# Kernel tuning notes

Measured on AMD Instinct MI355X. Metric: run time of the kernel, lower is better.

Reference implementation:

```python
import jax, jax.numpy as jnp
import numpy as np

NUM_FIELDS = 26

def setup_inputs() -> dict:
    key = jax.random.key(0)
    ks = jax.random.split(key, 8)
    B, F, D, V, d, af = 4096, NUM_FIELDS, 13, 100000, 64, 64
    return {
        "sparse_feat": jax.random.randint(ks[0], (B, F), 0, V, dtype=jnp.int32),
        "dense_feat": jax.random.uniform(ks[1], (B, D), dtype=jnp.float32),
        "embed_table": jax.random.normal(ks[2], (V, d), dtype=jnp.float32) * 0.05,
        "lin_table": jax.random.normal(ks[3], (V,), dtype=jnp.float32) * 0.05,
        "w_dense": jax.random.normal(ks[4], (D,), dtype=jnp.float32) * 0.1,
        "bias": jnp.zeros((1,), dtype=jnp.float32),
        "W1": jax.random.normal(ks[5], (d, af), dtype=jnp.float32) * (1.0 / np.sqrt(d)),
        "b1": jnp.zeros((af,), dtype=jnp.float32),
        "w2": jax.random.normal(ks[6], (af,), dtype=jnp.float32) * (1.0 / np.sqrt(af)),
        "p": jax.random.normal(ks[7], (d,), dtype=jnp.float32) * (1.0 / np.sqrt(d)),
    }

def reference(sparse_feat, dense_feat, embed_table, lin_table, w_dense, bias, W1, b1, w2, p):
    # Embedding lookup: [B, F, d]
    emb = embed_table[sparse_feat]
    # Linear part: per-field scalar weights + dense linear + bias -> [B]
    linear_out = lin_table[sparse_feat].sum(axis=1) + dense_feat @ w_dense + bias[0]
    # Pairwise interactions i<j (static indices): [B, P, d]
    i_idx, j_idx = np.triu_indices(NUM_FIELDS, k=1)
    att_x = emb[:, i_idx, :] * emb[:, j_idx, :]
    # Attention MLP: Linear(d, af) + ReLU + Linear(af, 1, no bias) -> [B, P]
    h = jax.nn.relu(jnp.einsum('bpd,da->bpa', att_x, W1) + b1)
    att_w = jnp.einsum('bpa,a->bp', h, w2)
    att_score = jax.nn.softmax(att_w, axis=1)
    # Softmax-weighted sum over pairs -> [B, d], then final projection p -> [B]
    att_out = jnp.einsum('bpd,bp->bd', att_x, att_score)
    fm_att_out = att_out @ p
    return linear_out + fm_att_out
```

## Files before the change

kernel.cpp:

```cpp
#include <hip/hip_runtime.h>
#include <math.h>


#define NF 26
#define NP 325
#define NMT 21
#define ED 64
#define AF 64
#define NDENSE 13
#define WPB 4
#define BLOCK (WPB * 64)
#define ESTRIDE 72
#define WSTRIDE 72

typedef __attribute__((ext_vector_type(8))) _Float16 half8;
typedef __attribute__((ext_vector_type(4))) float f32x4;

__device__ __forceinline__ half8 bcast8(float v) {
    _Float16 hh = (_Float16)v;
    half8 r = { hh, hh, hh, hh, hh, hh, hh, hh };
    return r;
}

__device__ __forceinline__ float qd_sum(float x) {
#if __has_builtin(__builtin_amdgcn_permlane16_swap) && __has_builtin(__builtin_amdgcn_permlane32_swap)
    {
        auto a = __builtin_amdgcn_permlane16_swap(__builtin_bit_cast(unsigned, x),
                                                  __builtin_bit_cast(unsigned, x),
                                                  false, false);
        x = __builtin_bit_cast(float, a[0]) + __builtin_bit_cast(float, a[1]);
        auto b = __builtin_amdgcn_permlane32_swap(__builtin_bit_cast(unsigned, x),
                                                  __builtin_bit_cast(unsigned, x),
                                                  false, false);
        x = __builtin_bit_cast(float, b[0]) + __builtin_bit_cast(float, b[1]);
    }
#else
    x += __shfl_xor(x, 16, 64);
    x += __shfl_xor(x, 32, 64);
#endif
    return x;
}

__global__ __launch_bounds__(BLOCK, 2)
void afm_kernel(const int*   __restrict__ sparse,
                const float* __restrict__ dense,
                const float* __restrict__ etab,
                const float* __restrict__ ltab,
                const float* __restrict__ wdense,
                const float* __restrict__ bias,
                const float* __restrict__ W1,
                const float* __restrict__ b1,
                const float* __restrict__ w2,
                const float* __restrict__ proj,
                float*       __restrict__ out,
                int B)
{
    const int t    = threadIdx.x;
    const int wave = t >> 6;
    const int lane = t & 63;
    const int qd   = lane >> 4;
    const int ln   = lane & 15;

    __shared__ alignas(16) _Float16       w1t_s[AF][WSTRIDE];
    __shared__              unsigned short tab_s[NMT * 16];
    __shared__ alignas(16) _Float16       emb_all[WPB][NF][ESTRIDE];

    for (int task = t; task < WPB * NF * 8; task += BLOCK) {
        int w   = task / (NF * 8);
        int rem = task - w * (NF * 8);
        int f = rem >> 3, c = rem & 7;
        int rw = blockIdx.x * WPB + w;
        if (rw < B) {
            const float* src = etab + (size_t)sparse[rw * NF + f] * ED + c * 8;
            float4 v0 = *(const float4*)(src);
            float4 v1 = *(const float4*)(src + 4);
            half8 hv = { (_Float16)v0.x, (_Float16)v0.y, (_Float16)v0.z, (_Float16)v0.w,
                         (_Float16)v1.x, (_Float16)v1.y, (_Float16)v1.z, (_Float16)v1.w };
            *(half8*)(&emb_all[w][f][c * 8]) = hv;
        }
    }
    for (int idx = t; idx < ED * AF; idx += BLOCK) {
        int d = idx >> 6, a = idx & 63;
        w1t_s[a][d] = (_Float16)W1[idx];
    }
    for (int p = t; p < NMT * 16; p += BLOCK) {
        unsigned short v = 0;
        if (p < NP) {
            int rem = p, i = 0;
            while (rem >= NF - 1 - i) { rem -= NF - 1 - i; ++i; }
            v = (unsigned short)(i | ((i + 1 + rem) << 8));
        }
        tab_s[p] = v;
    }

    const int r = blockIdx.x * WPB + wave;
    const bool active = (r < B);

    _Float16 (* __restrict__ emb)[ESTRIDE] = emb_all[wave];

    __syncthreads();
    if (!active) return;

    float4 b1v4[4], w2v4[4];
    #pragma unroll
    for (int nt = 0; nt < 4; ++nt) {
        b1v4[nt] = *(const float4*)(b1 + nt * 16 + qd * 4);
        w2v4[nt] = *(const float4*)(w2 + nt * 16 + qd * 4);
    }

    half8 bfr[4][2];
    #pragma unroll
    for (int nt = 0; nt < 4; ++nt)
        #pragma unroll
        for (int kh = 0; kh < 2; ++kh)
            bfr[nt][kh] = *(const half8*)(&w1t_s[nt * 16 + ln][kh * 32 + qd * 8]);

    float m = -INFINITY, l = 0.f;
    half8 acc0 = bcast8(0.f), acc1 = bcast8(0.f);

    {
        unsigned pp = tab_s[ln];
        int fi = pp & 0xff, fj = pp >> 8;
        (void)fi; (void)fj;
    }
    unsigned pp0 = tab_s[ln];
    int fi0 = pp0 & 0xff, fj0 = pp0 >> 8;
    half8 eiR0 = *(const half8*)(&emb[fi0][qd * 8]);
    half8 eiR1 = *(const half8*)(&emb[fi0][32 + qd * 8]);
    half8 ejR0 = *(const half8*)(&emb[fj0][qd * 8]);
    half8 ejR1 = *(const half8*)(&emb[fj0][32 + qd * 8]);

    float lgP = 0.f;
    half8 xP0 = bcast8(0.f), xP1 = bcast8(0.f);

    for (int k = 0; k < NMT; ++k) {
        half8 xC0 = eiR0 * ejR0;
        half8 xC1 = eiR1 * ejR1;

        if (k + 1 < NMT) {
            unsigned np = tab_s[(k + 1) * 16 + ln];
            int nfi = np & 0xff, nfj = np >> 8;
            eiR0 = *(const half8*)(&emb[nfi][qd * 8]);
            eiR1 = *(const half8*)(&emb[nfi][32 + qd * 8]);
            ejR0 = *(const half8*)(&emb[nfj][qd * 8]);
            ejR1 = *(const half8*)(&emb[nfj][32 + qd * 8]);
        }

        float lgp[4];
        #pragma unroll
        for (int nt = 0; nt < 4; ++nt) {
            f32x4 acc = { b1v4[nt].x, b1v4[nt].y, b1v4[nt].z, b1v4[nt].w };
            acc = __builtin_amdgcn_mfma_f32_16x16x32_f16(bfr[nt][0], xC0, acc, 0, 0, 0);
            acc = __builtin_amdgcn_mfma_f32_16x16x32_f16(bfr[nt][1], xC1, acc, 0, 0, 0);
            float u = fmaf(fmaxf(acc[1], 0.f), w2v4[nt].y, fmaxf(acc[0], 0.f) * w2v4[nt].x);
            float v = fmaf(fmaxf(acc[3], 0.f), w2v4[nt].w, fmaxf(acc[2], 0.f) * w2v4[nt].z);
            lgp[nt] = u + v;
        }
        float lg = (lgp[0] + lgp[1]) + (lgp[2] + lgp[3]);
        lg = qd_sum(lg);
        if (k * 16 + ln >= NP) lg = -INFINITY;

        if (k > 0) {
            float mn    = fmaxf(m, lgP);
            float alpha = __expf(m - mn);
            float e     = __expf(lgP - mn);
            l = l * alpha + e;
            m = mn;
            half8 a8 = bcast8(alpha), e8 = bcast8(e);
            acc0 = acc0 * a8 + xP0 * e8;
            acc1 = acc1 * a8 + xP1 * e8;
        }
        xP0 = xC0; xP1 = xC1; lgP = lg;
    }
    {
        float mn    = fmaxf(m, lgP);
        float alpha = __expf(m - mn);
        float e     = __expf(lgP - mn);
        l = l * alpha + e;
        m = mn;
        half8 a8 = bcast8(alpha), e8 = bcast8(e);
        acc0 = acc0 * a8 + xP0 * e8;
        acc1 = acc1 * a8 + xP1 * e8;
    }

    float lin = 0.f;
    if (lane < NF) {
        lin = ltab[sparse[r * NF + lane]];
    } else if (lane >= 32 && lane < 32 + NDENSE) {
        int k = lane - 32;
        lin = dense[r * NDENSE + k] * wdense[k];
    }
    #pragma unroll
    for (int off = 32; off >= 1; off >>= 1) lin += __shfl_xor(lin, off, 64);
    lin += bias[0];

    float mg = m;
    #pragma unroll
    for (int off = 1; off <= 8; off <<= 1) mg = fmaxf(mg, __shfl_xor(mg, off, 64));
    const float fac = __expf(m - mg);
    float lsum = l * fac;
    #pragma unroll
    for (int off = 1; off <= 8; off <<= 1) lsum += __shfl_xor(lsum, off, 64);

    float4 pa4 = *(const float4*)(proj + qd * 8);
    float4 pb4 = *(const float4*)(proj + qd * 8 + 4);
    float4 pc4 = *(const float4*)(proj + 32 + qd * 8);
    float4 pd4 = *(const float4*)(proj + 32 + qd * 8 + 4);
    float rr = (float)acc0[0] * pa4.x + (float)acc0[1] * pa4.y
             + (float)acc0[2] * pa4.z + (float)acc0[3] * pa4.w
             + (float)acc0[4] * pb4.x + (float)acc0[5] * pb4.y
             + (float)acc0[6] * pb4.z + (float)acc0[7] * pb4.w
             + (float)acc1[0] * pc4.x + (float)acc1[1] * pc4.y
             + (float)acc1[2] * pc4.z + (float)acc1[3] * pc4.w
             + (float)acc1[4] * pd4.x + (float)acc1[5] * pd4.y
             + (float)acc1[6] * pd4.z + (float)acc1[7] * pd4.w;
    rr *= fac;
    #pragma unroll
    for (int off = 1; off <= 32; off <<= 1) rr += __shfl_xor(rr, off, 64);

    if (lane == 0) out[r] = lin + rr / lsum;
}

extern "C" void kernel_launch(void* const* d_in, const int* in_sizes, int n_in,
                              void* d_out, int out_size, void* d_ws, size_t ws_size,
                              hipStream_t stream) {
    const int*   sparse = (const int*)  d_in[0];
    const float* dense  = (const float*)d_in[1];
    const float* etab   = (const float*)d_in[2];
    const float* ltab   = (const float*)d_in[3];
    const float* wdense = (const float*)d_in[4];
    const float* bias   = (const float*)d_in[5];
    const float* W1     = (const float*)d_in[6];
    const float* b1     = (const float*)d_in[7];
    const float* w2     = (const float*)d_in[8];
    const float* proj   = (const float*)d_in[9];
    float* outp = (float*)d_out;

    const int B = in_sizes[0] / NF;

    afm_kernel<<<dim3((B + WPB - 1) / WPB), dim3(BLOCK), 0, stream>>>(
        sparse, dense, etab, ltab, wdense, bias, W1, b1, w2, proj, outp, B);
    (void)n_in; (void)out_size; (void)d_ws; (void)ws_size;
}
```

Before: 110.4 us.

## Split each row's pair tiles across two waves with shared-memory softmax merge

Each block now handles two rows instead of four, and each row's 325 pairs are split between two waves (11 tiles each). Each wave keeps its own online-softmax state, and the two partial results are merged through shared memory after a block barrier. This halves the serial tile loop per wave and doubles the grid size, giving more latency hiding. The cost is an extra __syncthreads, reloading W1 into shared memory for twice as many blocks, and one extra padded tile.

```diff
diff --git a/kernel.cpp b/kernel.cpp
--- a/kernel.cpp
+++ b/kernel.cpp
@@ -4,10 +4,12 @@
 
 #define NF 26
 #define NP 325
-#define NMT 21
+#define NHT 11
+#define NTILE 22
 #define ED 64
 #define AF 64
 #define NDENSE 13
+#define RPB 2
 #define WPB 4
 #define BLOCK (WPB * 64)
 #define ESTRIDE 72
@@ -60,16 +62,19 @@
     const int lane = t & 63;
     const int qd   = lane >> 4;
     const int ln   = lane & 15;
+    const int lr   = wave >> 1;
+    const int h    = wave & 1;
 
     __shared__ alignas(16) _Float16       w1t_s[AF][WSTRIDE];
-    __shared__              unsigned short tab_s[NMT * 16];
-    __shared__ alignas(16) _Float16       emb_all[WPB][NF][ESTRIDE];
-
-    for (int task = t; task < WPB * NF * 8; task += BLOCK) {
+    __shared__              unsigned short tab_s[NTILE * 16];
+    __shared__ alignas(16) _Float16       emb_all[RPB][NF][ESTRIDE];
+    __shared__              float          red_s[WPB][4];
+
+    for (int task = t; task < RPB * NF * 8; task += BLOCK) {
         int w   = task / (NF * 8);
         int rem = task - w * (NF * 8);
         int f = rem >> 3, c = rem & 7;
-        int rw = blockIdx.x * WPB + w;
+        int rw = blockIdx.x * RPB + w;
         if (rw < B) {
             const float* src = etab + (size_t)sparse[rw * NF + f] * ED + c * 8;
             float4 v0 = *(const float4*)(src);
@@ -83,7 +88,7 @@
         int d = idx >> 6, a = idx & 63;
         w1t_s[a][d] = (_Float16)W1[idx];
     }
-    for (int p = t; p < NMT * 16; p += BLOCK) {
+    for (int p = t; p < NTILE * 16; p += BLOCK) {
         unsigned short v = 0;
         if (p < NP) {
             int rem = p, i = 0;
@@ -93,74 +98,83 @@
         tab_s[p] = v;
     }
 
-    const int r = blockIdx.x * WPB + wave;
+    const int r = blockIdx.x * RPB + lr;
     const bool active = (r < B);
 
-    _Float16 (* __restrict__ emb)[ESTRIDE] = emb_all[wave];
+    _Float16 (* __restrict__ emb)[ESTRIDE] = emb_all[lr];
+    float lin = 0.f;
 
     __syncthreads();
-    if (!active) return;
-
-    float4 b1v4[4], w2v4[4];
-    #pragma unroll
-    for (int nt = 0; nt < 4; ++nt) {
-        b1v4[nt] = *(const float4*)(b1 + nt * 16 + qd * 4);
-        w2v4[nt] = *(const float4*)(w2 + nt * 16 + qd * 4);
-    }
-
-    half8 bfr[4][2];
-    #pragma unroll
-    for (int nt = 0; nt < 4; ++nt)
-        #pragma unroll
-        for (int kh = 0; kh < 2; ++kh)
-            bfr[nt][kh] = *(const half8*)(&w1t_s[nt * 16 + ln][kh * 32 + qd * 8]);
-
-    float m = -INFINITY, l = 0.f;
-    half8 acc0 = bcast8(0.f), acc1 = bcast8(0.f);
-
-    {
-        unsigned pp = tab_s[ln];
-        int fi = pp & 0xff, fj = pp >> 8;
-        (void)fi; (void)fj;
-    }
-    unsigned pp0 = tab_s[ln];
-    int fi0 = pp0 & 0xff, fj0 = pp0 >> 8;
-    half8 eiR0 = *(const half8*)(&emb[fi0][qd * 8]);
-    half8 eiR1 = *(const half8*)(&emb[fi0][32 + qd * 8]);
-    half8 ejR0 = *(const half8*)(&emb[fj0][qd * 8]);
-    half8 ejR1 = *(const half8*)(&emb[fj0][32 + qd * 8]);
-
-    float lgP = 0.f;
-    half8 xP0 = bcast8(0.f), xP1 = bcast8(0.f);
-
-    for (int k = 0; k < NMT; ++k) {
-        half8 xC0 = eiR0 * ejR0;
-        half8 xC1 = eiR1 * ejR1;
-
-        if (k + 1 < NMT) {
-            unsigned np = tab_s[(k + 1) * 16 + ln];
-            int nfi = np & 0xff, nfj = np >> 8;
-            eiR0 = *(const half8*)(&emb[nfi][qd * 8]);
-            eiR1 = *(const half8*)(&emb[nfi][32 + qd * 8]);
-            ejR0 = *(const half8*)(&emb[nfj][qd * 8]);
-            ejR1 = *(const half8*)(&emb[nfj][32 + qd * 8]);
-        }
-
-        float lgp[4];
+
+    if (active) {
+        float4 b1v4[4], w2v4[4];
         #pragma unroll
         for (int nt = 0; nt < 4; ++nt) {
-            f32x4 acc = { b1v4[nt].x, b1v4[nt].y, b1v4[nt].z, b1v4[nt].w };
-            acc = __builtin_amdgcn_mfma_f32_16x16x32_f16(bfr[nt][0], xC0, acc, 0, 0, 0);
-            acc = __builtin_amdgcn_mfma_f32_16x16x32_f16(bfr[nt][1], xC1, acc, 0, 0, 0);
-            float u = fmaf(fmaxf(acc[1], 0.f), w2v4[nt].y, fmaxf(acc[0], 0.f) * w2v4[nt].x);
-            float v = fmaf(fmaxf(acc[3], 0.f), w2v4[nt].w, fmaxf(acc[2], 0.f) * w2v4[nt].z);
-            lgp[nt] = u + v;
-        }
-        float lg = (lgp[0] + lgp[1]) + (lgp[2] + lgp[3]);
-        lg = qd_sum(lg);
-        if (k * 16 + ln >= NP) lg = -INFINITY;
-
-        if (k > 0) {
+            b1v4[nt] = *(const float4*)(b1 + nt * 16 + qd * 4);
+            w2v4[nt] = *(const float4*)(w2 + nt * 16 + qd * 4);
+        }
+
+        half8 bfr[4][2];
+        #pragma unroll
+        for (int nt = 0; nt < 4; ++nt)
+            #pragma unroll
+            for (int kh = 0; kh < 2; ++kh)
+                bfr[nt][kh] = *(const half8*)(&w1t_s[nt * 16 + ln][kh * 32 + qd * 8]);
+
+        const int tbase = h * NHT;
+        float m = -INFINITY, l = 0.f;
+        half8 acc0 = bcast8(0.f), acc1 = bcast8(0.f);
+
+        unsigned pp0 = tab_s[tbase * 16 + ln];
+        int fi0 = pp0 & 0xff, fj0 = pp0 >> 8;
+        half8 eiR0 = *(const half8*)(&emb[fi0][qd * 8]);
+        half8 eiR1 = *(const half8*)(&emb[fi0][32 + qd * 8]);
+        half8 ejR0 = *(const half8*)(&emb[fj0][qd * 8]);
+        half8 ejR1 = *(const half8*)(&emb[fj0][32 + qd * 8]);
+
+        float lgP = 0.f;
+        half8 xP0 = bcast8(0.f), xP1 = bcast8(0.f);
+
+        for (int k = 0; k < NHT; ++k) {
+            half8 xC0 = eiR0 * ejR0;
+            half8 xC1 = eiR1 * ejR1;
+
+            if (k + 1 < NHT) {
+                unsigned np = tab_s[(tbase + k + 1) * 16 + ln];
+                int nfi = np & 0xff, nfj = np >> 8;
+                eiR0 = *(const half8*)(&emb[nfi][qd * 8]);
+                eiR1 = *(const half8*)(&emb[nfi][32 + qd * 8]);
+                ejR0 = *(const half8*)(&emb[nfj][qd * 8]);
+                ejR1 = *(const half8*)(&emb[nfj][32 + qd * 8]);
+            }
+
+            float lgp[4];
+            #pragma unroll
+            for (int nt = 0; nt < 4; ++nt) {
+                f32x4 acc = { b1v4[nt].x, b1v4[nt].y, b1v4[nt].z, b1v4[nt].w };
+                acc = __builtin_amdgcn_mfma_f32_16x16x32_f16(bfr[nt][0], xC0, acc, 0, 0, 0);
+                acc = __builtin_amdgcn_mfma_f32_16x16x32_f16(bfr[nt][1], xC1, acc, 0, 0, 0);
+                float u = fmaf(fmaxf(acc[1], 0.f), w2v4[nt].y, fmaxf(acc[0], 0.f) * w2v4[nt].x);
+                float v = fmaf(fmaxf(acc[3], 0.f), w2v4[nt].w, fmaxf(acc[2], 0.f) * w2v4[nt].z);
+                lgp[nt] = u + v;
+            }
+            float lg = (lgp[0] + lgp[1]) + (lgp[2] + lgp[3]);
+            lg = qd_sum(lg);
+            if ((tbase + k) * 16 + ln >= NP) lg = -INFINITY;
+
+            if (k > 0) {
+                float mn    = fmaxf(m, lgP);
+                float alpha = __expf(m - mn);
+                float e     = __expf(lgP - mn);
+                l = l * alpha + e;
+                m = mn;
+                half8 a8 = bcast8(alpha), e8 = bcast8(e);
+                acc0 = acc0 * a8 + xP0 * e8;
+                acc1 = acc1 * a8 + xP1 * e8;
+            }
+            xP0 = xC0; xP1 = xC1; lgP = lg;
+        }
+        {
             float mn    = fmaxf(m, lgP);
             float alpha = __expf(m - mn);
             float e     = __expf(lgP - mn);
@@ -170,55 +184,59 @@
             acc0 = acc0 * a8 + xP0 * e8;
             acc1 = acc1 * a8 + xP1 * e8;
         }
-        xP0 = xC0; xP1 = xC1; lgP = lg;
-    }
-    {
-        float mn    = fmaxf(m, lgP);
-        float alpha = __expf(m - mn);
-        float e     = __expf(lgP - mn);
-        l = l * alpha + e;
-        m = mn;
-        half8 a8 = bcast8(alpha), e8 = bcast8(e);
-        acc0 = acc0 * a8 + xP0 * e8;
-        acc1 = acc1 * a8 + xP1 * e8;
-    }
-
-    float lin = 0.f;
-    if (lane < NF) {
-        lin = ltab[sparse[r * NF + lane]];
-    } else if (lane >= 32 && lane < 32 + NDENSE) {
-        int k = lane - 32;
-        lin = dense[r * NDENSE + k] * wdense[k];
-    }
-    #pragma unroll
-    for (int off = 32; off >= 1; off >>= 1) lin += __shfl_xor(lin, off, 64);
-    lin += bias[0];
-
-    float mg = m;
-    #pragma unroll
-    for (int off = 1; off <= 8; off <<= 1) mg = fmaxf(mg, __shfl_xor(mg, off, 64));
-    const float fac = __expf(m - mg);
-    float lsum = l * fac;
-    #pragma unroll
-    for (int off = 1; off <= 8; off <<= 1) lsum += __shfl_xor(lsum, off, 64);
-
-    float4 pa4 = *(const float4*)(proj + qd * 8);
-    float4 pb4 = *(const float4*)(proj + qd * 8 + 4);
-    float4 pc4 = *(const float4*)(proj + 32 + qd * 8);
-    float4 pd4 = *(const float4*)(proj + 32 + qd * 8 + 4);
-    float rr = (float)acc0[0] * pa4.x + (float)acc0[1] * pa4.y
-             + (float)acc0[2] * pa4.z + (float)acc0[3] * pa4.w
-             + (float)acc0[4] * pb4.x + (float)acc0[5] * pb4.y
-             + (float)acc0[6] * pb4.z + (float)acc0[7] * pb4.w
-             + (float)acc1[0] * pc4.x + (float)acc1[1] * pc4.y
-             + (float)acc1[2] * pc4.z + (float)acc1[3] * pc4.w
-             + (float)acc1[4] * pd4.x + (float)acc1[5] * pd4.y
-             + (float)acc1[6] * pd4.z + (float)acc1[7] * pd4.w;
-    rr *= fac;
-    #pragma unroll
-    for (int off = 1; off <= 32; off <<= 1) rr += __shfl_xor(rr, off, 64);
-
-    if (lane == 0) out[r] = lin + rr / lsum;
+
+        float mg = m;
+        #pragma unroll
+        for (int off = 1; off <= 8; off <<= 1) mg = fmaxf(mg, __shfl_xor(mg, off, 64));
+        const float fac = __expf(m - mg);
+        float lsum = l * fac;
+        #pragma unroll
+        for (int off = 1; off <= 8; off <<= 1) lsum += __shfl_xor(lsum, off, 64);
+
+        float4 pa4 = *(const float4*)(proj + qd * 8);
+        float4 pb4 = *(const float4*)(proj + qd * 8 + 4);
+        float4 pc4 = *(const float4*)(proj + 32 + qd * 8);
+        float4 pd4 = *(const float4*)(proj + 32 + qd * 8 + 4);
+        float rr = (float)acc0[0] * pa4.x + (float)acc0[1] * pa4.y
+                 + (float)acc0[2] * pa4.z + (float)acc0[3] * pa4.w
+                 + (float)acc0[4] * pb4.x + (float)acc0[5] * pb4.y
+                 + (float)acc0[6] * pb4.z + (float)acc0[7] * pb4.w
+                 + (float)acc1[0] * pc4.x + (float)acc1[1] * pc4.y
+                 + (float)acc1[2] * pc4.z + (float)acc1[3] * pc4.w
+                 + (float)acc1[4] * pd4.x + (float)acc1[5] * pd4.y
+                 + (float)acc1[6] * pd4.z + (float)acc1[7] * pd4.w;
+        rr *= fac;
+        #pragma unroll
+        for (int off = 1; off <= 32; off <<= 1) rr += __shfl_xor(rr, off, 64);
+
+        if (lane == 0) {
+            red_s[wave][0] = mg;
+            red_s[wave][1] = lsum;
+            red_s[wave][2] = rr;
+        }
+
+        if (h == 0) {
+            if (lane < NF) {
+                lin = ltab[sparse[r * NF + lane]];
+            } else if (lane >= 32 && lane < 32 + NDENSE) {
+                int k = lane - 32;
+                lin = dense[r * NDENSE + k] * wdense[k];
+            }
+            #pragma unroll
+            for (int off = 32; off >= 1; off >>= 1) lin += __shfl_xor(lin, off, 64);
+            lin += bias[0];
+        }
+    }
+
+    __syncthreads();
+
+    if (active && h == 0 && lane == 0) {
+        float m0 = red_s[wave][0],     l0 = red_s[wave][1],     r0 = red_s[wave][2];
+        float m1 = red_s[wave + 1][0], l1 = red_s[wave + 1][1], r1 = red_s[wave + 1][2];
+        float mg = fmaxf(m0, m1);
+        float f0 = __expf(m0 - mg), f1 = __expf(m1 - mg);
+        out[r] = lin + (r0 * f0 + r1 * f1) / (l0 * f0 + l1 * f1);
+    }
 }
 
 extern "C" void kernel_launch(void* const* d_in, const int* in_sizes, int n_in,
@@ -238,7 +256,7 @@
 
     const int B = in_sizes[0] / NF;
 
-    afm_kernel<<<dim3((B + WPB - 1) / WPB), dim3(BLOCK), 0, stream>>>(
+    afm_kernel<<<dim3((B + RPB - 1) / RPB), dim3(BLOCK), 0, stream>>>(
         sparse, dense, etab, ltab, wdense, bias, W1, b1, w2, proj, outp, B);
     (void)n_in; (void)out_size; (void)d_ws; (void)ws_size;
 }
```

New measurement: 113.4 us. 1.03x slower.

## Replace online softmax with two-pass softmax over register-held logits

Applied to the files above, without the earlier changes.

Drops the streaming online-softmax recurrence (running max, rescale of the accumulators each step). The loop is fully unrolled and all 21 logits are kept in registers, then the kernel does a global max, a batch of exps with split partial sums, and a second pass that recomputes the pair products from LDS and accumulates them into two interleaved half8 accumulators. This removes the serial dependency chain and the per-step rescaling, at the cost of reloading the embeddings from LDS a second time and higher register pressure under launch_bounds(256,2).

```diff
diff --git a/kernel.cpp b/kernel.cpp
--- a/kernel.cpp
+++ b/kernel.cpp
@@ -115,73 +115,69 @@
         for (int kh = 0; kh < 2; ++kh)
             bfr[nt][kh] = *(const half8*)(&w1t_s[nt * 16 + ln][kh * 32 + qd * 8]);
 
-    float m = -INFINITY, l = 0.f;
-    half8 acc0 = bcast8(0.f), acc1 = bcast8(0.f);
-
-    {
-        unsigned pp = tab_s[ln];
+    float lg[NMT];
+    #pragma unroll
+    for (int k = 0; k < NMT; ++k) {
+        unsigned pp = tab_s[k * 16 + ln];
         int fi = pp & 0xff, fj = pp >> 8;
-        (void)fi; (void)fj;
-    }
-    unsigned pp0 = tab_s[ln];
-    int fi0 = pp0 & 0xff, fj0 = pp0 >> 8;
-    half8 eiR0 = *(const half8*)(&emb[fi0][qd * 8]);
-    half8 eiR1 = *(const half8*)(&emb[fi0][32 + qd * 8]);
-    half8 ejR0 = *(const half8*)(&emb[fj0][qd * 8]);
-    half8 ejR1 = *(const half8*)(&emb[fj0][32 + qd * 8]);
-
-    float lgP = 0.f;
-    half8 xP0 = bcast8(0.f), xP1 = bcast8(0.f);
-
-    for (int k = 0; k < NMT; ++k) {
-        half8 xC0 = eiR0 * ejR0;
-        half8 xC1 = eiR1 * ejR1;
-
-        if (k + 1 < NMT) {
-            unsigned np = tab_s[(k + 1) * 16 + ln];
-            int nfi = np & 0xff, nfj = np >> 8;
-            eiR0 = *(const half8*)(&emb[nfi][qd * 8]);
-            eiR1 = *(const half8*)(&emb[nfi][32 + qd * 8]);
-            ejR0 = *(const half8*)(&emb[nfj][qd * 8]);
-            ejR1 = *(const half8*)(&emb[nfj][32 + qd * 8]);
-        }
+        half8 x0 = *(const half8*)(&emb[fi][qd * 8])      * *(const half8*)(&emb[fj][qd * 8]);
+        half8 x1 = *(const half8*)(&emb[fi][32 + qd * 8]) * *(const half8*)(&emb[fj][32 + qd * 8]);
 
         float lgp[4];
         #pragma unroll
         for (int nt = 0; nt < 4; ++nt) {
             f32x4 acc = { b1v4[nt].x, b1v4[nt].y, b1v4[nt].z, b1v4[nt].w };
-            acc = __builtin_amdgcn_mfma_f32_16x16x32_f16(bfr[nt][0], xC0, acc, 0, 0, 0);
-            acc = __builtin_amdgcn_mfma_f32_16x16x32_f16(bfr[nt][1], xC1, acc, 0, 0, 0);
+            acc = __builtin_amdgcn_mfma_f32_16x16x32_f16(bfr[nt][0], x0, acc, 0, 0, 0);
+            acc = __builtin_amdgcn_mfma_f32_16x16x32_f16(bfr[nt][1], x1, acc, 0, 0, 0);
             float u = fmaf(fmaxf(acc[1], 0.f), w2v4[nt].y, fmaxf(acc[0], 0.f) * w2v4[nt].x);
             float v = fmaf(fmaxf(acc[3], 0.f), w2v4[nt].w, fmaxf(acc[2], 0.f) * w2v4[nt].z);
             lgp[nt] = u + v;
         }
-        float lg = (lgp[0] + lgp[1]) + (lgp[2] + lgp[3]);
-        lg = qd_sum(lg);
-        if (k * 16 + ln >= NP) lg = -INFINITY;
-
-        if (k > 0) {
-            float mn    = fmaxf(m, lgP);
-            float alpha = __expf(m - mn);
-            float e     = __expf(lgP - mn);
-            l = l * alpha + e;
-            m = mn;
-            half8 a8 = bcast8(alpha), e8 = bcast8(e);
-            acc0 = acc0 * a8 + xP0 * e8;
-            acc1 = acc1 * a8 + xP1 * e8;
-        }
-        xP0 = xC0; xP1 = xC1; lgP = lg;
-    }
-    {
-        float mn    = fmaxf(m, lgP);
-        float alpha = __expf(m - mn);
-        float e     = __expf(lgP - mn);
-        l = l * alpha + e;
-        m = mn;
-        half8 a8 = bcast8(alpha), e8 = bcast8(e);
-        acc0 = acc0 * a8 + xP0 * e8;
-        acc1 = acc1 * a8 + xP1 * e8;
-    }
+        float s = (lgp[0] + lgp[1]) + (lgp[2] + lgp[3]);
+        s = qd_sum(s);
+        lg[k] = (k * 16 + ln >= NP) ? -INFINITY : s;
+    }
+
+    float mA = lg[0], mB = lg[1], mC = lg[2], mD = lg[3];
+    #pragma unroll
+    for (int k = 4; k + 3 < NMT; k += 4) {
+        mA = fmaxf(mA, lg[k]);
+        mB = fmaxf(mB, lg[k + 1]);
+        mC = fmaxf(mC, lg[k + 2]);
+        mD = fmaxf(mD, lg[k + 3]);
+    }
+    mA = fmaxf(mA, lg[20]);
+    float mx = fmaxf(fmaxf(mA, mB), fmaxf(mC, mD));
+    #pragma unroll
+    for (int off = 1; off <= 8; off <<= 1) mx = fmaxf(mx, __shfl_xor(mx, off, 64));
+
+    float sA = 0.f, sB = 0.f, sC = 0.f, sD = 0.f;
+    #pragma unroll
+    for (int k = 0; k + 3 < NMT; k += 4) {
+        lg[k]     = __expf(lg[k]     - mx);  sA += lg[k];
+        lg[k + 1] = __expf(lg[k + 1] - mx);  sB += lg[k + 1];
+        lg[k + 2] = __expf(lg[k + 2] - mx);  sC += lg[k + 2];
+        lg[k + 3] = __expf(lg[k + 3] - mx);  sD += lg[k + 3];
+    }
+    lg[20] = __expf(lg[20] - mx);  sA += lg[20];
+    float lsum = (sA + sB) + (sC + sD);
+    #pragma unroll
+    for (int off = 1; off <= 8; off <<= 1) lsum += __shfl_xor(lsum, off, 64);
+
+    half8 accA0 = bcast8(0.f), accA1 = bcast8(0.f);
+    half8 accB0 = bcast8(0.f), accB1 = bcast8(0.f);
+    #pragma unroll
+    for (int k = 0; k < NMT; ++k) {
+        unsigned pp = tab_s[k * 16 + ln];
+        int fi = pp & 0xff, fj = pp >> 8;
+        half8 x0 = *(const half8*)(&emb[fi][qd * 8])      * *(const half8*)(&emb[fj][qd * 8]);
+        half8 x1 = *(const half8*)(&emb[fi][32 + qd * 8]) * *(const half8*)(&emb[fj][32 + qd * 8]);
+        half8 e8 = bcast8(lg[k]);
+        if (k & 1) { accB0 = accB0 + x0 * e8; accB1 = accB1 + x1 * e8; }
+        else       { accA0 = accA0 + x0 * e8; accA1 = accA1 + x1 * e8; }
+    }
+    half8 acc0 = accA0 + accB0;
+    half8 acc1 = accA1 + accB1;
 
     float lin = 0.f;
     if (lane < NF) {
@@ -193,14 +189,6 @@
     #pragma unroll
     for (int off = 32; off >= 1; off >>= 1) lin += __shfl_xor(lin, off, 64);
     lin += bias[0];
-
-    float mg = m;
-    #pragma unroll
-    for (int off = 1; off <= 8; off <<= 1) mg = fmaxf(mg, __shfl_xor(mg, off, 64));
-    const float fac = __expf(m - mg);
-    float lsum = l * fac;
-    #pragma unroll
-    for (int off = 1; off <= 8; off <<= 1) lsum += __shfl_xor(lsum, off, 64);
 
     float4 pa4 = *(const float4*)(proj + qd * 8);
     float4 pb4 = *(const float4*)(proj + qd * 8 + 4);
@@ -214,7 +202,6 @@
              + (float)acc1[2] * pc4.z + (float)acc1[3] * pc4.w
              + (float)acc1[4] * pd4.x + (float)acc1[5] * pd4.y
              + (float)acc1[6] * pd4.z + (float)acc1[7] * pd4.w;
-    rr *= fac;
     #pragma unroll
     for (int off = 1; off <= 32; off <<= 1) rr += __shfl_xor(rr, off, 64);
 
```

Result: slower. 117.2 us (+6.1%).

## Process two batch rows per wave to amortize W1 setup and interleave MFMA chains

Applied to the files above, without the earlier changes.

Each wave now handles two batch rows instead of one, so a block covers eight rows and half as many blocks are launched. The per-block W1 transpose into shared memory and the per-wave B-fragment register loads are amortized over twice as many rows. The two rows run as independent MFMA and online-softmax chains that can hide each other's latency. In exchange, register pressure and shared memory per block roughly double, which may lower occupancy, and the grid has fewer blocks.

```diff
diff --git a/kernel.cpp b/kernel.cpp
--- a/kernel.cpp
+++ b/kernel.cpp
@@ -8,7 +8,9 @@
 #define ED 64
 #define AF 64
 #define NDENSE 13
+#define RPW 2
 #define WPB 4
+#define RPB (WPB * RPW)
 #define BLOCK (WPB * 64)
 #define ESTRIDE 72
 #define WSTRIDE 72
@@ -63,13 +65,13 @@
 
     __shared__ alignas(16) _Float16       w1t_s[AF][WSTRIDE];
     __shared__              unsigned short tab_s[NMT * 16];
-    __shared__ alignas(16) _Float16       emb_all[WPB][NF][ESTRIDE];
-
-    for (int task = t; task < WPB * NF * 8; task += BLOCK) {
+    __shared__ alignas(16) _Float16       emb_all[RPB][NF][ESTRIDE];
+
+    for (int task = t; task < RPB * NF * 8; task += BLOCK) {
         int w   = task / (NF * 8);
         int rem = task - w * (NF * 8);
         int f = rem >> 3, c = rem & 7;
-        int rw = blockIdx.x * WPB + w;
+        int rw = blockIdx.x * RPB + w;
         if (rw < B) {
             const float* src = etab + (size_t)sparse[rw * NF + f] * ED + c * 8;
             float4 v0 = *(const float4*)(src);
@@ -93,13 +95,16 @@
         tab_s[p] = v;
     }
 
-    const int r = blockIdx.x * WPB + wave;
-    const bool active = (r < B);
-
-    _Float16 (* __restrict__ emb)[ESTRIDE] = emb_all[wave];
+    const int rA = blockIdx.x * RPB + wave * RPW;
+    const int rB = rA + 1;
+    const bool actA = (rA < B);
+    const bool actB = (rB < B);
+
+    _Float16 (* __restrict__ embA)[ESTRIDE] = emb_all[wave * RPW];
+    _Float16 (* __restrict__ embB)[ESTRIDE] = emb_all[wave * RPW + (actB ? 1 : 0)];
 
     __syncthreads();
-    if (!active) return;
+    if (!actA) return;
 
     float4 b1v4[4], w2v4[4];
     #pragma unroll
@@ -115,110 +120,171 @@
         for (int kh = 0; kh < 2; ++kh)
             bfr[nt][kh] = *(const half8*)(&w1t_s[nt * 16 + ln][kh * 32 + qd * 8]);
 
-    float m = -INFINITY, l = 0.f;
-    half8 acc0 = bcast8(0.f), acc1 = bcast8(0.f);
-
-    {
-        unsigned pp = tab_s[ln];
-        int fi = pp & 0xff, fj = pp >> 8;
-        (void)fi; (void)fj;
-    }
+    float mA = -INFINITY, lA = 0.f;
+    float mB = -INFINITY, lB = 0.f;
+    half8 accA0 = bcast8(0.f), accA1 = bcast8(0.f);
+    half8 accB0 = bcast8(0.f), accB1 = bcast8(0.f);
+
     unsigned pp0 = tab_s[ln];
     int fi0 = pp0 & 0xff, fj0 = pp0 >> 8;
-    half8 eiR0 = *(const half8*)(&emb[fi0][qd * 8]);
-    half8 eiR1 = *(const half8*)(&emb[fi0][32 + qd * 8]);
-    half8 ejR0 = *(const half8*)(&emb[fj0][qd * 8]);
-    half8 ejR1 = *(const half8*)(&emb[fj0][32 + qd * 8]);
-
-    float lgP = 0.f;
-    half8 xP0 = bcast8(0.f), xP1 = bcast8(0.f);
+    half8 eiA0 = *(const half8*)(&embA[fi0][qd * 8]);
+    half8 eiA1 = *(const half8*)(&embA[fi0][32 + qd * 8]);
+    half8 ejA0 = *(const half8*)(&embA[fj0][qd * 8]);
+    half8 ejA1 = *(const half8*)(&embA[fj0][32 + qd * 8]);
+    half8 eiB0 = *(const half8*)(&embB[fi0][qd * 8]);
+    half8 eiB1 = *(const half8*)(&embB[fi0][32 + qd * 8]);
+    half8 ejB0 = *(const half8*)(&embB[fj0][qd * 8]);
+    half8 ejB1 = *(const half8*)(&embB[fj0][32 + qd * 8]);
+
+    float lgPA = 0.f, lgPB = 0.f;
+    half8 xPA0 = bcast8(0.f), xPA1 = bcast8(0.f);
+    half8 xPB0 = bcast8(0.f), xPB1 = bcast8(0.f);
 
     for (int k = 0; k < NMT; ++k) {
-        half8 xC0 = eiR0 * ejR0;
-        half8 xC1 = eiR1 * ejR1;
+        half8 xA0 = eiA0 * ejA0;
+        half8 xA1 = eiA1 * ejA1;
+        half8 xB0 = eiB0 * ejB0;
+        half8 xB1 = eiB1 * ejB1;
 
         if (k + 1 < NMT) {
             unsigned np = tab_s[(k + 1) * 16 + ln];
             int nfi = np & 0xff, nfj = np >> 8;
-            eiR0 = *(const half8*)(&emb[nfi][qd * 8]);
-            eiR1 = *(const half8*)(&emb[nfi][32 + qd * 8]);
-            ejR0 = *(const half8*)(&emb[nfj][qd * 8]);
-            ejR1 = *(const half8*)(&emb[nfj][32 + qd * 8]);
-        }
-
-        float lgp[4];
+            eiA0 = *(const half8*)(&embA[nfi][qd * 8]);
+            eiA1 = *(const half8*)(&embA[nfi][32 + qd * 8]);
+            ejA0 = *(const half8*)(&embA[nfj][qd * 8]);
+            ejA1 = *(const half8*)(&embA[nfj][32 + qd * 8]);
+            eiB0 = *(const half8*)(&embB[nfi][qd * 8]);
+            eiB1 = *(const half8*)(&embB[nfi][32 + qd * 8]);
+            ejB0 = *(const half8*)(&embB[nfj][qd * 8]);
+            ejB1 = *(const half8*)(&embB[nfj][32 + qd * 8]);
+        }
+
+        float lgpA[4], lgpB[4];
         #pragma unroll
         for (int nt = 0; nt < 4; ++nt) {
-            f32x4 acc = { b1v4[nt].x, b1v4[nt].y, b1v4[nt].z, b1v4[nt].w };
-            acc = __builtin_amdgcn_mfma_f32_16x16x32_f16(bfr[nt][0], xC0, acc, 0, 0, 0);
-            acc = __builtin_amdgcn_mfma_f32_16x16x32_f16(bfr[nt][1], xC1, acc, 0, 0, 0);
-            float u = fmaf(fmaxf(acc[1], 0.f), w2v4[nt].y, fmaxf(acc[0], 0.f) * w2v4[nt].x);
-            float v = fmaf(fmaxf(acc[3], 0.f), w2v4[nt].w, fmaxf(acc[2], 0.f) * w2v4[nt].z);
-            lgp[nt] = u + v;
-        }
-        float lg = (lgp[0] + lgp[1]) + (lgp[2] + lgp[3]);
-        lg = qd_sum(lg);
-        if (k * 16 + ln >= NP) lg = -INFINITY;
+            f32x4 ca = { b1v4[nt].x, b1v4[nt].y, b1v4[nt].z, b1v4[nt].w };
+            ca = __builtin_amdgcn_mfma_f32_16x16x32_f16(bfr[nt][0], xA0, ca, 0, 0, 0);
+            ca = __builtin_amdgcn_mfma_f32_16x16x32_f16(bfr[nt][1], xA1, ca, 0, 0, 0);
+            f32x4 cb = { b1v4[nt].x, b1v4[nt].y, b1v4[nt].z, b1v4[nt].w };
+            cb = __builtin_amdgcn_mfma_f32_16x16x32_f16(bfr[nt][0], xB0, cb, 0, 0, 0);
+            cb = __builtin_amdgcn_mfma_f32_16x16x32_f16(bfr[nt][1], xB1, cb, 0, 0, 0);
+            float ua = fmaf(fmaxf(ca[1], 0.f), w2v4[nt].y, fmaxf(ca[0], 0.f) * w2v4[nt].x);
+            float va = fmaf(fmaxf(ca[3], 0.f), w2v4[nt].w, fmaxf(ca[2], 0.f) * w2v4[nt].z);
+            lgpA[nt] = ua + va;
+            float ub = fmaf(fmaxf(cb[1], 0.f), w2v4[nt].y, fmaxf(cb[0], 0.f) * w2v4[nt].x);
+            float vb = fmaf(fmaxf(cb[3], 0.f), w2v4[nt].w, fmaxf(cb[2], 0.f) * w2v4[nt].z);
+            lgpB[nt] = ub + vb;
+        }
+        float lgA = (lgpA[0] + lgpA[1]) + (lgpA[2] + lgpA[3]);
+        float lgB = (lgpB[0] + lgpB[1]) + (lgpB[2] + lgpB[3]);
+        lgA = qd_sum(lgA);
+        lgB = qd_sum(lgB);
+        if (k * 16 + ln >= NP) { lgA = -INFINITY; lgB = -INFINITY; }
 
         if (k > 0) {
-            float mn    = fmaxf(m, lgP);
-            float alpha = __expf(m - mn);
-            float e     = __expf(lgP - mn);
-            l = l * alpha + e;
-            m = mn;
-            half8 a8 = bcast8(alpha), e8 = bcast8(e);
-            acc0 = acc0 * a8 + xP0 * e8;
-            acc1 = acc1 * a8 + xP1 * e8;
-        }
-        xP0 = xC0; xP1 = xC1; lgP = lg;
+            float mnA    = fmaxf(mA, lgPA);
+            float mnB    = fmaxf(mB, lgPB);
+            float alphaA = __expf(mA - mnA);
+            float alphaB = __expf(mB - mnB);
+            float eA     = __expf(lgPA - mnA);
+            float eB     = __expf(lgPB - mnB);
+            lA = lA * alphaA + eA;
+            lB = lB * alphaB + eB;
+            mA = mnA;
+            mB = mnB;
+            half8 a8A = bcast8(alphaA), e8A = bcast8(eA);
+            half8 a8B = bcast8(alphaB), e8B = bcast8(eB);
+            accA0 = accA0 * a8A + xPA0 * e8A;
+            accA1 = accA1 * a8A + xPA1 * e8A;
+            accB0 = accB0 * a8B + xPB0 * e8B;
+            accB1 = accB1 * a8B + xPB1 * e8B;
+        }
+        xPA0 = xA0; xPA1 = xA1; lgPA = lgA;
+        xPB0 = xB0; xPB1 = xB1; lgPB = lgB;
     }
     {
-        float mn    = fmaxf(m, lgP);
-        float alpha = __expf(m - mn);
-        float e     = __expf(lgP - mn);
-        l = l * alpha + e;
-        m = mn;
-        half8 a8 = bcast8(alpha), e8 = bcast8(e);
-        acc0 = acc0 * a8 + xP0 * e8;
-        acc1 = acc1 * a8 + xP1 * e8;
-    }
-
-    float lin = 0.f;
-    if (lane < NF) {
-        lin = ltab[sparse[r * NF + lane]];
-    } else if (lane >= 32 && lane < 32 + NDENSE) {
-        int k = lane - 32;
-        lin = dense[r * NDENSE + k] * wdense[k];
-    }
-    #pragma unroll
-    for (int off = 32; off >= 1; off >>= 1) lin += __shfl_xor(lin, off, 64);
-    lin += bias[0];
-
-    float mg = m;
-    #pragma unroll
-    for (int off = 1; off <= 8; off <<= 1) mg = fmaxf(mg, __shfl_xor(mg, off, 64));
-    const float fac = __expf(m - mg);
-    float lsum = l * fac;
-    #pragma unroll
-    for (int off = 1; off <= 8; off <<= 1) lsum += __shfl_xor(lsum, off, 64);
+        float mnA    = fmaxf(mA, lgPA);
+        float mnB    = fmaxf(mB, lgPB);
+        float alphaA = __expf(mA - mnA);
+        float alphaB = __expf(mB - mnB);
+        float eA     = __expf(lgPA - mnA);
+        float eB     = __expf(lgPB - mnB);
+        lA = lA * alphaA + eA;
+        lB = lB * alphaB + eB;
+        mA = mnA;
+        mB = mnB;
+        half8 a8A = bcast8(alphaA), e8A = bcast8(eA);
+        half8 a8B = bcast8(alphaB), e8B = bcast8(eB);
+        accA0 = accA0 * a8A + xPA0 * e8A;
+        accA1 = accA1 * a8A + xPA1 * e8A;
+        accB0 = accB0 * a8B + xPB0 * e8B;
+        accB1 = accB1 * a8B + xPB1 * e8B;
+    }
+
+    float mgA = mA, mgB = mB;
+    #pragma unroll
+    for (int off = 1; off <= 8; off <<= 1) {
+        mgA = fmaxf(mgA, __shfl_xor(mgA, off, 64));
+        mgB = fmaxf(mgB, __shfl_xor(mgB, off, 64));
+    }
+    const float facA = __expf(mA - mgA);
+    const float facB = __expf(mB - mgB);
+    float lsumA = lA * facA, lsumB = lB * facB;
+    #pragma unroll
+    for (int off = 1; off <= 8; off <<= 1) {
+        lsumA += __shfl_xor(lsumA, off, 64);
+        lsumB += __shfl_xor(lsumB, off, 64);
+    }
 
     float4 pa4 = *(const float4*)(proj + qd * 8);
     float4 pb4 = *(const float4*)(proj + qd * 8 + 4);
     float4 pc4 = *(const float4*)(proj + 32 + qd * 8);
     float4 pd4 = *(const float4*)(proj + 32 + qd * 8 + 4);
-    float rr = (float)acc0[0] * pa4.x + (float)acc0[1] * pa4.y
-             + (float)acc0[2] * pa4.z + (float)acc0[3] * pa4.w
-             + (float)acc0[4] * pb4.x + (float)acc0[5] * pb4.y
-             + (float)acc0[6] * pb4.z + (float)acc0[7] * pb4.w
-             + (float)acc1[0] * pc4.x + (float)acc1[1] * pc4.y
-             + (float)acc1[2] * pc4.z + (float)acc1[3] * pc4.w
-             + (float)acc1[4] * pd4.x + (float)acc1[5] * pd4.y
-             + (float)acc1[6] * pd4.z + (float)acc1[7] * pd4.w;
-    rr *= fac;
-    #pragma unroll
-    for (int off = 1; off <= 32; off <<= 1) rr += __shfl_xor(rr, off, 64);
-
-    if (lane == 0) out[r] = lin + rr / lsum;
+    float rrA = (float)accA0[0] * pa4.x + (float)accA0[1] * pa4.y
+              + (float)accA0[2] * pa4.z + (float)accA0[3] * pa4.w
+              + (float)accA0[4] * pb4.x + (float)accA0[5] * pb4.y
+              + (float)accA0[6] * pb4.z + (float)accA0[7] * pb4.w
+              + (float)accA1[0] * pc4.x + (float)accA1[1] * pc4.y
+              + (float)accA1[2] * pc4.z + (float)accA1[3] * pc4.w
+              + (float)accA1[4] * pd4.x + (float)accA1[5] * pd4.y
+              + (float)accA1[6] * pd4.z + (float)accA1[7] * pd4.w;
+    float rrB = (float)accB0[0] * pa4.x + (float)accB0[1] * pa4.y
+              + (float)accB0[2] * pa4.z + (float)accB0[3] * pa4.w
+              + (float)accB0[4] * pb4.x + (float)accB0[5] * pb4.y
+              + (float)accB0[6] * pb4.z + (float)accB0[7] * pb4.w
+              + (float)accB1[0] * pc4.x + (float)accB1[1] * pc4.y
+              + (float)accB1[2] * pc4.z + (float)accB1[3] * pc4.w
+              + (float)accB1[4] * pd4.x + (float)accB1[5] * pd4.y
+              + (float)accB1[6] * pd4.z + (float)accB1[7] * pd4.w;
+    rrA *= facA;
+    rrB *= facB;
+    #pragma unroll
+    for (int off = 1; off <= 32; off <<= 1) {
+        rrA += __shfl_xor(rrA, off, 64);
+        rrB += __shfl_xor(rrB, off, 64);
+    }
+
+    float linA = 0.f, linB = 0.f;
+    if (lane < NF) {
+        linA = ltab[sparse[rA * NF + lane]];
+        if (actB) linB = ltab[sparse[rB * NF + lane]];
+    } else if (lane >= 32 && lane < 32 + NDENSE) {
+        int k = lane - 32;
+        linA = dense[rA * NDENSE + k] * wdense[k];
+        if (actB) linB = dense[rB * NDENSE + k] * wdense[k];
+    }
+    #pragma unroll
+    for (int off = 32; off >= 1; off >>= 1) {
+        linA += __shfl_xor(linA, off, 64);
+        linB += __shfl_xor(linB, off, 64);
+    }
+    linA += bias[0];
+    linB += bias[0];
+
+    if (lane == 0) {
+        out[rA] = linA + rrA / lsumA;
+        if (actB) out[rB] = linB + rrB / lsumB;
+    }
 }
 
 extern "C" void kernel_launch(void* const* d_in, const int* in_sizes, int n_in,
@@ -238,7 +304,7 @@
 
     const int B = in_sizes[0] / NF;
 
-    afm_kernel<<<dim3((B + WPB - 1) / WPB), dim3(BLOCK), 0, stream>>>(
+    afm_kernel<<<dim3((B + RPB - 1) / RPB), dim3(BLOCK), 0, stream>>>(
         sparse, dense, etab, ltab, wdense, bias, W1, b1, w2, proj, outp, B);
     (void)n_in; (void)out_size; (void)d_ws; (void)ws_size;
 }
```

Result: slower. 113.2 us (+2.5%).
